# Kernel optimization log

Hardware: AMD Instinct MI355X
Metric: run time of the kernel (lower is better)

## Reference

```python
import jax, jax.numpy as jnp
import numpy as np

D_M, D_K, D_V, HEADS = 1024, 64, 64, 16
B, S = 2, 2048


def setup_inputs() -> dict:
    key = jax.random.key(0)
    ks = jax.random.split(key, 5)
    x = jax.random.normal(ks[0], (B, S, D_M), dtype=jnp.float32)
    # per-head projection weights (original deep-copies one rand init per head;
    # we give each head independent weights, matching the per-head param structure)
    Wk = jax.random.uniform(ks[1], (HEADS, D_M, D_K), dtype=jnp.float32)
    Wq = jax.random.uniform(ks[2], (HEADS, D_M, D_K), dtype=jnp.float32)
    Wv = jax.random.uniform(ks[3], (HEADS, D_M, D_V), dtype=jnp.float32)
    Wo = jax.random.uniform(ks[4], (HEADS * D_V, D_M), dtype=jnp.float32)
    return {"x": x, "Wk": Wk, "Wq": Wq, "Wv": Wv, "Wo": Wo}


def reference(x, Wk, Wq, Wv, Wo):
    # per-head QKV projections, batched over heads: [B,H,S,d]
    q = jnp.einsum("bsm,hmk->bhsk", x, Wq)
    k = jnp.einsum("bsm,hmk->bhsk", x, Wk)
    v = jnp.einsum("bsm,hmv->bhsv", x, Wv)
    scale = 1.0 / jnp.sqrt(jnp.asarray(q.shape[-1], dtype=q.dtype))
    scores = jnp.einsum("bhsk,bhtk->bhst", q, k) * scale  # [B,H,S,S]
    attn = jax.nn.softmax(scores, axis=-1)
    ctx = jnp.einsum("bhst,bhtv->bhsv", attn, v)  # [B,H,S,d_v]
    # concat heads -> [B,S,H*d_v], then output projection
    ctx = jnp.transpose(ctx, (0, 2, 1, 3)).reshape(x.shape[0], x.shape[1], -1)
    return jnp.einsum("bsc,cm->bsm", ctx, Wo)
```

## Files before the change

kernel.cpp:

```cpp
#include <hip/hip_runtime.h>
#include <hip/hip_bf16.h>
#include <stdint.h>

#define DM   1024
#define DKV  64
#define HEADS 16
#define BATCH 2
#define SEQ  2048
#define BS   (BATCH*SEQ)
#define BHD  (BATCH*HEADS)

typedef __attribute__((ext_vector_type(8))) short bf16x8;
typedef __attribute__((ext_vector_type(4))) short bf16x4;
typedef __attribute__((ext_vector_type(4))) float f32x4;

__device__ inline unsigned fb(float f) { union { float f; unsigned u; } v; v.f = f; return v.u; }

__device__ inline unsigned short bf16_rtn(float f) {
  unsigned u = fb(f);
  unsigned r = u + 0x7fffu + ((u >> 16) & 1u);
  return (unsigned short)(r >> 16);
}
__device__ inline float bf16_to_f(unsigned short h) {
  union { unsigned u; float f; } v; v.u = ((unsigned)h) << 16; return v.f;
}
__device__ inline void split_bf16(float x, unsigned short& hi, unsigned short& lo) {
  hi = bf16_rtn(x);
  lo = bf16_rtn(x - bf16_to_f(hi));
}
__device__ inline unsigned pack2_bf16(float lo_elem, float hi_elem) {
  return __builtin_amdgcn_perm(fb(hi_elem) + 0x8000u, fb(lo_elem) + 0x8000u, 0x07060302u);
}

__device__ inline float fast_exp2(float x) {
#if __has_builtin(__builtin_amdgcn_exp2f)
  return __builtin_amdgcn_exp2f(x);
#else
  return exp2f(x);
#endif
}

__device__ inline f32x4 mfma16x16x16_bf16(bf16x4 a, bf16x4 b, f32x4 c) {
#if __has_builtin(__builtin_amdgcn_mfma_f32_16x16x16bf16_1k)
  return __builtin_amdgcn_mfma_f32_16x16x16bf16_1k(a, b, c, 0, 0, 0);
#else
  asm volatile("v_mfma_f32_16x16x16_bf16 %0, %1, %2, %0" : "+v"(c) : "v"(a), "v"(b));
  return c;
#endif
}

__device__ inline void stage16(const unsigned short* g, unsigned short* lds_base, int lane) {
#if __has_builtin(__builtin_amdgcn_global_load_lds)
  __builtin_amdgcn_global_load_lds((__attribute__((address_space(1))) void*)(g),
                                   (__attribute__((address_space(3))) void*)(lds_base),
                                   16, 0, 0);
#else
  *(bf16x8*)(lds_base + lane * 8) = *(const bf16x8*)g;
#endif
}

__device__ inline int swz(int row, int chunk) {
  return row * 64 + (((chunk ^ (row & 7)) & 7) << 3);
}

__global__ void cvt_x_split(const float* __restrict__ x,
                            unsigned short* __restrict__ xh, unsigned short* __restrict__ xl) {
  int i = (blockIdx.x * 256 + threadIdx.x) * 8;
  bf16x8 oh, ol;
  #pragma unroll
  for (int j = 0; j < 8; ++j) {
    unsigned short hi, lo;
    split_bf16(x[i + j], hi, lo);
    oh[j] = (short)hi; ol[j] = (short)lo;
  }
  *(bf16x8*)(xh + i) = oh;
  *(bf16x8*)(xl + i) = ol;
}

__global__ void pack_qkv_split(const float* __restrict__ Wq, const float* __restrict__ Wk,
                               const float* __restrict__ Wv,
                               unsigned short* __restrict__ Wh, unsigned short* __restrict__ Wl) {
  __shared__ float tile[64][65];
  int bid = blockIdx.x;
  int p = bid >> 8, h = (bid >> 4) & 15, mt = bid & 15;
  const float* W = (p == 0) ? Wq : (p == 1) ? Wk : Wv;
  const float* src = W + (size_t)h * (DM * DKV);
  int t = threadIdx.x;
  int m0 = mt * 64;
  #pragma unroll
  for (int pass = 0; pass < 16; ++pass) {
    int row = pass * 4 + (t >> 6), col = t & 63;
    tile[row][col] = src[(size_t)(m0 + row) * DKV + col];
  }
  __syncthreads();
  int cbase = p * 1024 + h * 64;
  #pragma unroll
  for (int pass = 0; pass < 16; ++pass) {
    int krow = pass * 4 + (t >> 6), mcol = t & 63;
    unsigned short hi, lo;
    split_bf16(tile[mcol][krow], hi, lo);
    size_t idx = (size_t)(cbase + krow) * DM + m0 + mcol;
    Wh[idx] = hi; Wl[idx] = lo;
  }
}

__global__ void pack_wo(const float* __restrict__ Wo, unsigned short* __restrict__ WoT) {
  __shared__ float tile[64][65];
  int ib = blockIdx.x >> 4, jb = blockIdx.x & 15;
  int t = threadIdx.x;
  #pragma unroll
  for (int pass = 0; pass < 16; ++pass) {
    int row = pass * 4 + (t >> 6), col = t & 63;
    tile[row][col] = Wo[(size_t)(ib * 64 + row) * DM + jb * 64 + col];
  }
  __syncthreads();
  #pragma unroll
  for (int pass = 0; pass < 16; ++pass) {
    int a = pass * 4 + (t >> 6), b = t & 63;
    WoT[(size_t)(jb * 64 + a) * DM + ib * 64 + b] = bf16_rtn(tile[b][a]);
  }
}

__global__ __launch_bounds__(256, 2)
void gemm_qk(const unsigned short* __restrict__ Ah, const unsigned short* __restrict__ Al,
             const unsigned short* __restrict__ Bh, const unsigned short* __restrict__ Bl,
             unsigned short* __restrict__ Qh, unsigned short* __restrict__ Ql,
             unsigned short* __restrict__ Kh, unsigned short* __restrict__ Kl) {
  __shared__ unsigned short AsH[128 * 32], AsL[128 * 32];
  __shared__ unsigned short BsH[128 * 32], BsL[128 * 32];
  const int tid = threadIdx.x;
  const int w = tid >> 6, lane = tid & 63;
  const int quad = lane >> 4, l16 = lane & 15;
  const int wm = w >> 1, wn = w & 1;
  const int bn = blockIdx.x, bm = blockIdx.y;

  f32x4 acc[4][4];
  #pragma unroll
  for (int i = 0; i < 4; ++i)
    #pragma unroll
    for (int j = 0; j < 4; ++j) acc[i][j] = (f32x4){0.f, 0.f, 0.f, 0.f};

  const int r4 = lane >> 2, c4 = lane & 3;
  const size_t offA = (size_t)(bm * 128 + w * 32 + r4) * DM + c4 * 8;
  const size_t offB = (size_t)(bn * 128 + w * 32 + r4) * DM + c4 * 8;
  unsigned short* lAh0 = AsH + (w * 32) * 32;      unsigned short* lAh1 = AsH + (w * 32 + 16) * 32;
  unsigned short* lAl0 = AsL + (w * 32) * 32;      unsigned short* lAl1 = AsL + (w * 32 + 16) * 32;
  unsigned short* lBh0 = BsH + (w * 32) * 32;      unsigned short* lBh1 = BsH + (w * 32 + 16) * 32;
  unsigned short* lBl0 = BsL + (w * 32) * 32;      unsigned short* lBl1 = BsL + (w * 32 + 16) * 32;

  for (int kk = 0; kk < DM / 32; ++kk) {
    stage16(Ah + offA + kk * 32,           lAh0, lane);
    stage16(Ah + offA + kk * 32 + 16 * DM, lAh1, lane);
    stage16(Al + offA + kk * 32,           lAl0, lane);
    stage16(Al + offA + kk * 32 + 16 * DM, lAl1, lane);
    stage16(Bh + offB + kk * 32,           lBh0, lane);
    stage16(Bh + offB + kk * 32 + 16 * DM, lBh1, lane);
    stage16(Bl + offB + kk * 32,           lBl0, lane);
    stage16(Bl + offB + kk * 32 + 16 * DM, lBl1, lane);
    asm volatile("s_waitcnt vmcnt(0)" ::: "memory");
    __syncthreads();
    bf16x8 afh[4], afl[4], bfh[4], bfl[4];
    #pragma unroll
    for (int mt = 0; mt < 4; ++mt) {
      afh[mt] = *(const bf16x8*)(AsH + (wm * 64 + mt * 16 + l16) * 32 + quad * 8);
      afl[mt] = *(const bf16x8*)(AsL + (wm * 64 + mt * 16 + l16) * 32 + quad * 8);
    }
    #pragma unroll
    for (int nt = 0; nt < 4; ++nt) {
      bfh[nt] = *(const bf16x8*)(BsH + (wn * 64 + nt * 16 + l16) * 32 + quad * 8);
      bfl[nt] = *(const bf16x8*)(BsL + (wn * 64 + nt * 16 + l16) * 32 + quad * 8);
    }
    #pragma unroll
    for (int mt = 0; mt < 4; ++mt)
      #pragma unroll
      for (int nt = 0; nt < 4; ++nt) {
        acc[mt][nt] = __builtin_amdgcn_mfma_f32_16x16x32_bf16(afh[mt], bfh[nt], acc[mt][nt], 0, 0, 0);
        acc[mt][nt] = __builtin_amdgcn_mfma_f32_16x16x32_bf16(afh[mt], bfl[nt], acc[mt][nt], 0, 0, 0);
        acc[mt][nt] = __builtin_amdgcn_mfma_f32_16x16x32_bf16(afl[mt], bfh[nt], acc[mt][nt], 0, 0, 0);
      }
    __syncthreads();
  }

  const float SCL = 0.18033688011112042f;
  #pragma unroll
  for (int mt = 0; mt < 4; ++mt) {
    int m_g = bm * 128 + wm * 64 + mt * 16 + quad * 4;
    #pragma unroll
    for (int nt = 0; nt < 4; ++nt) {
      int n_g = bn * 128 + wn * 64 + nt * 16 + l16;
      int p = n_g >> 10, h = (n_g >> 6) & 15, k = n_g & 63;
      #pragma unroll
      for (int r = 0; r < 4; ++r) {
        int row = m_g + r;
        int b = row >> 11, s = row & 2047;
        int bh = b * HEADS + h;
        float v = acc[mt][nt][r];
        size_t idx = ((size_t)(bh * SEQ + s)) * DKV + k;
        unsigned short hi, lo;
        if (p == 0) {
          split_bf16(v * SCL, hi, lo);
          Qh[idx] = hi; Ql[idx] = lo;
        } else {
          split_bf16(v, hi, lo);
          Kh[idx] = hi; Kl[idx] = lo;
        }
      }
    }
  }
}

__global__ __launch_bounds__(256, 2)
void gemm_v(const unsigned short* __restrict__ A, const unsigned short* __restrict__ Bt,
            unsigned short* __restrict__ Vt) {
  __shared__ unsigned short As[128 * 32];
  __shared__ unsigned short Bs[128 * 32];
  const int tid = threadIdx.x;
  const int w = tid >> 6, lane = tid & 63;
  const int quad = lane >> 4, l16 = lane & 15;
  const int wm = w >> 1, wn = w & 1;
  const int bn = blockIdx.x, bm = blockIdx.y;

  f32x4 acc[4][4];
  #pragma unroll
  for (int i = 0; i < 4; ++i)
    #pragma unroll
    for (int j = 0; j < 4; ++j) acc[i][j] = (f32x4){0.f, 0.f, 0.f, 0.f};

  const int r4 = lane >> 2, c4 = lane & 3;
  const unsigned short* gA0 = A  + (size_t)(bm * 128 + w * 32 + r4) * DM + c4 * 8;
  const unsigned short* gB0 = Bt + (size_t)(bn * 128 + w * 32 + r4) * DM + c4 * 8;
  unsigned short* lA0 = As + (w * 32) * 32;
  unsigned short* lA1 = As + (w * 32 + 16) * 32;
  unsigned short* lB0 = Bs + (w * 32) * 32;
  unsigned short* lB1 = Bs + (w * 32 + 16) * 32;

  for (int kk = 0; kk < DM / 32; ++kk) {
    stage16(gA0 + kk * 32,           lA0, lane);
    stage16(gA0 + kk * 32 + 16 * DM, lA1, lane);
    stage16(gB0 + kk * 32,           lB0, lane);
    stage16(gB0 + kk * 32 + 16 * DM, lB1, lane);
    asm volatile("s_waitcnt vmcnt(0)" ::: "memory");
    __syncthreads();
    bf16x8 af[4], bfr[4];
    #pragma unroll
    for (int mt = 0; mt < 4; ++mt)
      af[mt] = *(const bf16x8*)(As + (wm * 64 + mt * 16 + l16) * 32 + quad * 8);
    #pragma unroll
    for (int nt = 0; nt < 4; ++nt)
      bfr[nt] = *(const bf16x8*)(Bs + (wn * 64 + nt * 16 + l16) * 32 + quad * 8);
    #pragma unroll
    for (int mt = 0; mt < 4; ++mt)
      #pragma unroll
      for (int nt = 0; nt < 4; ++nt)
        acc[mt][nt] = __builtin_amdgcn_mfma_f32_16x16x32_bf16(af[mt], bfr[nt], acc[mt][nt], 0, 0, 0);
    __syncthreads();
  }

  #pragma unroll
  for (int mt = 0; mt < 4; ++mt) {
    int m_g = bm * 128 + wm * 64 + mt * 16 + quad * 4;
    #pragma unroll
    for (int nt = 0; nt < 4; ++nt) {
      int n_g = bn * 128 + wn * 64 + nt * 16 + l16;
      int h = n_g >> 6, k = n_g & 63;
      #pragma unroll
      for (int r = 0; r < 4; ++r) {
        int row = m_g + r;
        int b = row >> 11, s = row & 2047;
        int bh = b * HEADS + h;
        Vt[((size_t)(bh * DKV + k)) * SEQ + s] = bf16_rtn(acc[mt][nt][r]);
      }
    }
  }
}

__global__ __launch_bounds__(256, 2)
void flash(const unsigned short* __restrict__ Qh, const unsigned short* __restrict__ Ql,
           const unsigned short* __restrict__ Kh, const unsigned short* __restrict__ Kl,
           const unsigned short* __restrict__ Vt, unsigned short* __restrict__ ctx) {
  __shared__ unsigned short KtH[64 * 64], KtL[64 * 64], Vts[64 * 64];
  const int tid = threadIdx.x;
  const int w = tid >> 6, lane = tid & 63, quad = lane >> 4, l16 = lane & 15;
  const int bh = blockIdx.x;
  const int q0 = blockIdx.y * 128;

  bf16x8 qfh[2][2], qfl[2][2];
  #pragma unroll
  for (int qt = 0; qt < 2; ++qt) {
    int qrow = q0 + w * 32 + qt * 16 + l16;
    size_t base = ((size_t)(bh * SEQ + qrow)) * DKV + quad * 8;
    qfh[qt][0] = *(const bf16x8*)(Qh + base);
    qfh[qt][1] = *(const bf16x8*)(Qh + base + 32);
    qfl[qt][0] = *(const bf16x8*)(Ql + base);
    qfl[qt][1] = *(const bf16x8*)(Ql + base + 32);
  }

  float m_run[2] = {-1e30f, -1e30f};
  float l_run[2] = {0.f, 0.f};
  f32x4 acc[2][4];
  #pragma unroll
  for (int qt = 0; qt < 2; ++qt)
    #pragma unroll
    for (int vt = 0; vt < 4; ++vt) acc[qt][vt] = (f32x4){0.f, 0.f, 0.f, 0.f};

  const int srow = tid >> 3, sc8 = tid & 7;

  bf16x8 rkh[2], rkl[2], rv[2];
  #pragma unroll
  for (int p = 0; p < 2; ++p) {
    int row = p * 32 + srow;
    size_t kidx = ((size_t)(bh * SEQ + row)) * DKV + sc8 * 8;
    rkh[p] = *(const bf16x8*)(Kh + kidx);
    rkl[p] = *(const bf16x8*)(Kl + kidx);
    rv[p]  = *(const bf16x8*)(Vt + ((size_t)(bh * DKV + row)) * SEQ + sc8 * 8);
  }

  for (int kt = 0; kt < SEQ / 64; ++kt) {
    __syncthreads();
    #pragma unroll
    for (int p = 0; p < 2; ++p) {
      int row = p * 32 + srow;
      int o = swz(row, sc8);
      *(bf16x8*)(KtH + o) = rkh[p];
      *(bf16x8*)(KtL + o) = rkl[p];
      *(bf16x8*)(Vts + o) = rv[p];
    }
    __syncthreads();
    if (kt + 1 < SEQ / 64) {
      int kt0 = (kt + 1) * 64;
      #pragma unroll
      for (int p = 0; p < 2; ++p) {
        int row = p * 32 + srow;
        size_t kidx = ((size_t)(bh * SEQ + kt0 + row)) * DKV + sc8 * 8;
        rkh[p] = *(const bf16x8*)(Kh + kidx);
        rkl[p] = *(const bf16x8*)(Kl + kidx);
        rv[p]  = *(const bf16x8*)(Vt + ((size_t)(bh * DKV + row)) * SEQ + kt0 + sc8 * 8);
      }
    }

    f32x4 st[4][2];
    #pragma unroll
    for (int mt = 0; mt < 4; ++mt) {
      int rowA = mt * 16 + l16;
      bf16x8 kah0 = *(const bf16x8*)(KtH + swz(rowA, quad));
      bf16x8 kah1 = *(const bf16x8*)(KtH + swz(rowA, quad + 4));
      bf16x8 kal0 = *(const bf16x8*)(KtL + swz(rowA, quad));
      bf16x8 kal1 = *(const bf16x8*)(KtL + swz(rowA, quad + 4));
      #pragma unroll
      for (int qt = 0; qt < 2; ++qt) {
        f32x4 c = (f32x4){0.f, 0.f, 0.f, 0.f};
        c = __builtin_amdgcn_mfma_f32_16x16x32_bf16(kah0, qfh[qt][0], c, 0, 0, 0);
        c = __builtin_amdgcn_mfma_f32_16x16x32_bf16(kah1, qfh[qt][1], c, 0, 0, 0);
        c = __builtin_amdgcn_mfma_f32_16x16x32_bf16(kah0, qfl[qt][0], c, 0, 0, 0);
        c = __builtin_amdgcn_mfma_f32_16x16x32_bf16(kah1, qfl[qt][1], c, 0, 0, 0);
        c = __builtin_amdgcn_mfma_f32_16x16x32_bf16(kal0, qfh[qt][0], c, 0, 0, 0);
        c = __builtin_amdgcn_mfma_f32_16x16x32_bf16(kal1, qfh[qt][1], c, 0, 0, 0);
        st[mt][qt] = c;
      }
    }

    bf16x4 pb[2][4];
    #pragma unroll
    for (int qt = 0; qt < 2; ++qt) {
      float cm = -1e30f;
      #pragma unroll
      for (int mt = 0; mt < 4; ++mt)
        #pragma unroll
        for (int r = 0; r < 4; ++r) cm = fmaxf(cm, st[mt][qt][r]);
      cm = fmaxf(cm, __shfl_xor(cm, 16));
      cm = fmaxf(cm, __shfl_xor(cm, 32));
      bool upd = cm > m_run[qt];
      float mn = upd ? cm : m_run[qt];
      float ssum = 0.f;
      #pragma unroll
      for (int mt = 0; mt < 4; ++mt) {
        float p0 = fast_exp2(st[mt][qt][0] - mn);
        float p1 = fast_exp2(st[mt][qt][1] - mn);
        float p2 = fast_exp2(st[mt][qt][2] - mn);
        float p3 = fast_exp2(st[mt][qt][3] - mn);
        ssum += (p0 + p1) + (p2 + p3);
        union { bf16x4 v; unsigned u2[2]; } pk;
        pk.u2[0] = pack2_bf16(p0, p1);
        pk.u2[1] = pack2_bf16(p2, p3);
        pb[qt][mt] = pk.v;
      }
      ssum += __shfl_xor(ssum, 16);
      ssum += __shfl_xor(ssum, 32);
      if (__ballot(upd)) {
        float alpha = fast_exp2(m_run[qt] - mn);
        m_run[qt] = mn;
        l_run[qt] = l_run[qt] * alpha + ssum;
        #pragma unroll
        for (int vt = 0; vt < 4; ++vt) acc[qt][vt] = acc[qt][vt] * alpha;
      } else {
        l_run[qt] += ssum;
      }
    }

    #pragma unroll
    for (int vt = 0; vt < 4; ++vt) {
      #pragma unroll
      for (int mt = 0; mt < 4; ++mt) {
        int row = vt * 16 + l16;
        int addr = row * 64 + ((((mt * 2 + (quad >> 1)) ^ (row & 7)) & 7) << 3) + (quad & 1) * 4;
        bf16x4 va = *(const bf16x4*)(Vts + addr);
        #pragma unroll
        for (int qt = 0; qt < 2; ++qt)
          acc[qt][vt] = mfma16x16x16_bf16(va, pb[qt][mt], acc[qt][vt]);
      }
    }
  }

  int h = bh & 15, b = bh >> 4;
  #pragma unroll
  for (int qt = 0; qt < 2; ++qt) {
    float inv = 1.0f / l_run[qt];
    int bs = b * SEQ + q0 + w * 32 + qt * 16 + l16;
    #pragma unroll
    for (int vt = 0; vt < 4; ++vt) {
      union { bf16x4 v; unsigned u2[2]; } pk;
      pk.u2[0] = pack2_bf16(acc[qt][vt][0] * inv, acc[qt][vt][1] * inv);
      pk.u2[1] = pack2_bf16(acc[qt][vt][2] * inv, acc[qt][vt][3] * inv);
      *(bf16x4*)(ctx + (size_t)bs * DM + h * 64 + vt * 16 + quad * 4) = pk.v;
    }
  }
}

__global__ __launch_bounds__(256, 2)
void gemm_out(const unsigned short* __restrict__ A, const unsigned short* __restrict__ Bt,
              float* __restrict__ out) {
  __shared__ unsigned short As[128 * 32];
  __shared__ unsigned short Bs[128 * 32];
  const int tid = threadIdx.x;
  const int w = tid >> 6, lane = tid & 63;
  const int quad = lane >> 4, l16 = lane & 15;
  const int wm = w >> 1, wn = w & 1;
  const int bn = blockIdx.x, bm = blockIdx.y;

  f32x4 acc[4][4];
  #pragma unroll
  for (int i = 0; i < 4; ++i)
    #pragma unroll
    for (int j = 0; j < 4; ++j) acc[i][j] = (f32x4){0.f, 0.f, 0.f, 0.f};

  const int r4 = lane >> 2, c4 = lane & 3;
  const unsigned short* gA0 = A  + (size_t)(bm * 128 + w * 32 + r4) * DM + c4 * 8;
  const unsigned short* gB0 = Bt + (size_t)(bn * 128 + w * 32 + r4) * DM + c4 * 8;
  unsigned short* lA0 = As + (w * 32) * 32;
  unsigned short* lA1 = As + (w * 32 + 16) * 32;
  unsigned short* lB0 = Bs + (w * 32) * 32;
  unsigned short* lB1 = Bs + (w * 32 + 16) * 32;

  for (int kk = 0; kk < DM / 32; ++kk) {
    stage16(gA0 + kk * 32,           lA0, lane);
    stage16(gA0 + kk * 32 + 16 * DM, lA1, lane);
    stage16(gB0 + kk * 32,           lB0, lane);
    stage16(gB0 + kk * 32 + 16 * DM, lB1, lane);
    asm volatile("s_waitcnt vmcnt(0)" ::: "memory");
    __syncthreads();
    bf16x8 af[4], bfr[4];
    #pragma unroll
    for (int mt = 0; mt < 4; ++mt)
      af[mt] = *(const bf16x8*)(As + (wm * 64 + mt * 16 + l16) * 32 + quad * 8);
    #pragma unroll
    for (int nt = 0; nt < 4; ++nt)
      bfr[nt] = *(const bf16x8*)(Bs + (wn * 64 + nt * 16 + l16) * 32 + quad * 8);
    #pragma unroll
    for (int mt = 0; mt < 4; ++mt)
      #pragma unroll
      for (int nt = 0; nt < 4; ++nt)
        acc[mt][nt] = __builtin_amdgcn_mfma_f32_16x16x32_bf16(af[mt], bfr[nt], acc[mt][nt], 0, 0, 0);
    __syncthreads();
  }

  #pragma unroll
  for (int mt = 0; mt < 4; ++mt) {
    int m_g = bm * 128 + wm * 64 + mt * 16 + quad * 4;
    #pragma unroll
    for (int nt = 0; nt < 4; ++nt) {
      int n_g = bn * 128 + wn * 64 + nt * 16 + l16;
      #pragma unroll
      for (int r = 0; r < 4; ++r)
        out[(size_t)(m_g + r) * DM + n_g] = acc[mt][nt][r];
    }
  }
}

extern "C" void kernel_launch(void* const* d_in, const int* in_sizes, int n_in,
                              void* d_out, int out_size, void* d_ws, size_t ws_size,
                              hipStream_t stream) {
  const float* x  = (const float*)d_in[0];
  const float* Wk = (const float*)d_in[1];
  const float* Wq = (const float*)d_in[2];
  const float* Wv = (const float*)d_in[3];
  const float* Wo = (const float*)d_in[4];
  float* out = (float*)d_out;

  unsigned short* xh  = (unsigned short*)d_ws;
  unsigned short* xl  = xh  + (size_t)BS * DM;
  unsigned short* Wh  = xl  + (size_t)BS * DM;
  unsigned short* Wl  = Wh  + (size_t)3 * DM * DM;
  unsigned short* WoT = Wl  + (size_t)3 * DM * DM;
  unsigned short* Qh  = WoT + (size_t)DM * DM;
  unsigned short* Ql  = Qh  + (size_t)BHD * SEQ * DKV;
  unsigned short* Kh  = Ql  + (size_t)BHD * SEQ * DKV;
  unsigned short* Kl  = Kh  + (size_t)BHD * SEQ * DKV;
  unsigned short* Vtb = Kl  + (size_t)BHD * SEQ * DKV;
  unsigned short* ctx = Vtb + (size_t)BHD * SEQ * DKV;

  cvt_x_split<<<(BS * DM) / (256 * 8), 256, 0, stream>>>(x, xh, xl);
  pack_qkv_split<<<3 * 16 * 16, 256, 0, stream>>>(Wq, Wk, Wv, Wh, Wl);
  pack_wo<<<16 * 16, 256, 0, stream>>>(Wo, WoT);
  gemm_qk<<<dim3(16, 32), 256, 0, stream>>>(xh, xl, Wh, Wl, Qh, Ql, Kh, Kl);
  gemm_v<<<dim3(8, 32), 256, 0, stream>>>(xh, Wh + (size_t)2048 * DM, Vtb);
  flash<<<dim3(BHD, SEQ / 128), 256, 0, stream>>>(Qh, Ql, Kh, Kl, Vtb, ctx);
  gemm_out<<<dim3(8, 32), 256, 0, stream>>>(ctx, WoT, out);
}
```

Before: 270.8 us.

## Load K and V MFMA fragments directly from global memory, dropping LDS staging

The flash kernel no longer stages K (hi/lo) and V tiles through shared memory with two barriers per iteration. Each wave now loads its own MFMA operand fragments for K and V straight from global memory into registers, prefetching the next tile after the current use. This removes the LDS writes, LDS reads and __syncthreads. In exchange, each of the four waves fetches the full K/V tile on its own, using fewer, narrower accesses, which multiplies global/L2 traffic and adds register pressure.

```diff
diff --git a/kernel.cpp b/kernel.cpp
--- a/kernel.cpp
+++ b/kernel.cpp
@@ -57,10 +57,6 @@
 #else
   *(bf16x8*)(lds_base + lane * 8) = *(const bf16x8*)g;
 #endif
-}
-
-__device__ inline int swz(int row, int chunk) {
-  return row * 64 + (((chunk ^ (row & 7)) & 7) << 3);
 }
 
 __global__ void cvt_x_split(const float* __restrict__ x,
@@ -278,7 +274,6 @@
 void flash(const unsigned short* __restrict__ Qh, const unsigned short* __restrict__ Ql,
            const unsigned short* __restrict__ Kh, const unsigned short* __restrict__ Kl,
            const unsigned short* __restrict__ Vt, unsigned short* __restrict__ ctx) {
-  __shared__ unsigned short KtH[64 * 64], KtL[64 * 64], Vts[64 * 64];
   const int tid = threadIdx.x;
   const int w = tid >> 6, lane = tid & 63, quad = lane >> 4, l16 = lane & 15;
   const int bh = blockIdx.x;
@@ -303,59 +298,52 @@
     #pragma unroll
     for (int vt = 0; vt < 4; ++vt) acc[qt][vt] = (f32x4){0.f, 0.f, 0.f, 0.f};
 
-  const int srow = tid >> 3, sc8 = tid & 7;
-
-  bf16x8 rkh[2], rkl[2], rv[2];
-  #pragma unroll
-  for (int p = 0; p < 2; ++p) {
-    int row = p * 32 + srow;
-    size_t kidx = ((size_t)(bh * SEQ + row)) * DKV + sc8 * 8;
-    rkh[p] = *(const bf16x8*)(Kh + kidx);
-    rkl[p] = *(const bf16x8*)(Kl + kidx);
-    rv[p]  = *(const bf16x8*)(Vt + ((size_t)(bh * DKV + row)) * SEQ + sc8 * 8);
-  }
+  const size_t krow0 = ((size_t)(bh * SEQ + l16)) * DKV + quad * 8;
+  const size_t vrow0 = ((size_t)(bh * DKV + l16)) * SEQ + quad * 4;
+
+  bf16x8 kfh[4][2], kfl[4][2];
+  bf16x4 vf[4][4];
+
+  #pragma unroll
+  for (int mt = 0; mt < 4; ++mt) {
+    size_t r = krow0 + (size_t)(mt * 16) * DKV;
+    kfh[mt][0] = *(const bf16x8*)(Kh + r);
+    kfh[mt][1] = *(const bf16x8*)(Kh + r + 32);
+    kfl[mt][0] = *(const bf16x8*)(Kl + r);
+    kfl[mt][1] = *(const bf16x8*)(Kl + r + 32);
+  }
+  #pragma unroll
+  for (int vt = 0; vt < 4; ++vt)
+    #pragma unroll
+    for (int mt = 0; mt < 4; ++mt)
+      vf[vt][mt] = *(const bf16x4*)(Vt + vrow0 + (size_t)(vt * 16) * SEQ + mt * 16);
 
   for (int kt = 0; kt < SEQ / 64; ++kt) {
-    __syncthreads();
-    #pragma unroll
-    for (int p = 0; p < 2; ++p) {
-      int row = p * 32 + srow;
-      int o = swz(row, sc8);
-      *(bf16x8*)(KtH + o) = rkh[p];
-      *(bf16x8*)(KtL + o) = rkl[p];
-      *(bf16x8*)(Vts + o) = rv[p];
-    }
-    __syncthreads();
-    if (kt + 1 < SEQ / 64) {
-      int kt0 = (kt + 1) * 64;
-      #pragma unroll
-      for (int p = 0; p < 2; ++p) {
-        int row = p * 32 + srow;
-        size_t kidx = ((size_t)(bh * SEQ + kt0 + row)) * DKV + sc8 * 8;
-        rkh[p] = *(const bf16x8*)(Kh + kidx);
-        rkl[p] = *(const bf16x8*)(Kl + kidx);
-        rv[p]  = *(const bf16x8*)(Vt + ((size_t)(bh * DKV + row)) * SEQ + kt0 + sc8 * 8);
-      }
-    }
-
     f32x4 st[4][2];
     #pragma unroll
     for (int mt = 0; mt < 4; ++mt) {
-      int rowA = mt * 16 + l16;
-      bf16x8 kah0 = *(const bf16x8*)(KtH + swz(rowA, quad));
-      bf16x8 kah1 = *(const bf16x8*)(KtH + swz(rowA, quad + 4));
-      bf16x8 kal0 = *(const bf16x8*)(KtL + swz(rowA, quad));
-      bf16x8 kal1 = *(const bf16x8*)(KtL + swz(rowA, quad + 4));
       #pragma unroll
       for (int qt = 0; qt < 2; ++qt) {
         f32x4 c = (f32x4){0.f, 0.f, 0.f, 0.f};
-        c = __builtin_amdgcn_mfma_f32_16x16x32_bf16(kah0, qfh[qt][0], c, 0, 0, 0);
-        c = __builtin_amdgcn_mfma_f32_16x16x32_bf16(kah1, qfh[qt][1], c, 0, 0, 0);
-        c = __builtin_amdgcn_mfma_f32_16x16x32_bf16(kah0, qfl[qt][0], c, 0, 0, 0);
-        c = __builtin_amdgcn_mfma_f32_16x16x32_bf16(kah1, qfl[qt][1], c, 0, 0, 0);
-        c = __builtin_amdgcn_mfma_f32_16x16x32_bf16(kal0, qfh[qt][0], c, 0, 0, 0);
-        c = __builtin_amdgcn_mfma_f32_16x16x32_bf16(kal1, qfh[qt][1], c, 0, 0, 0);
+        c = __builtin_amdgcn_mfma_f32_16x16x32_bf16(kfh[mt][0], qfh[qt][0], c, 0, 0, 0);
+        c = __builtin_amdgcn_mfma_f32_16x16x32_bf16(kfh[mt][1], qfh[qt][1], c, 0, 0, 0);
+        c = __builtin_amdgcn_mfma_f32_16x16x32_bf16(kfh[mt][0], qfl[qt][0], c, 0, 0, 0);
+        c = __builtin_amdgcn_mfma_f32_16x16x32_bf16(kfh[mt][1], qfl[qt][1], c, 0, 0, 0);
+        c = __builtin_amdgcn_mfma_f32_16x16x32_bf16(kfl[mt][0], qfh[qt][0], c, 0, 0, 0);
+        c = __builtin_amdgcn_mfma_f32_16x16x32_bf16(kfl[mt][1], qfh[qt][1], c, 0, 0, 0);
         st[mt][qt] = c;
+      }
+    }
+
+    if (kt + 1 < SEQ / 64) {
+      size_t kbase = krow0 + (size_t)((kt + 1) * 64) * DKV;
+      #pragma unroll
+      for (int mt = 0; mt < 4; ++mt) {
+        size_t r = kbase + (size_t)(mt * 16) * DKV;
+        kfh[mt][0] = *(const bf16x8*)(Kh + r);
+        kfh[mt][1] = *(const bf16x8*)(Kh + r + 32);
+        kfl[mt][0] = *(const bf16x8*)(Kl + r);
+        kfl[mt][1] = *(const bf16x8*)(Kl + r + 32);
       }
     }
 
@@ -398,16 +386,20 @@
     }
 
     #pragma unroll
-    for (int vt = 0; vt < 4; ++vt) {
-      #pragma unroll
-      for (int mt = 0; mt < 4; ++mt) {
-        int row = vt * 16 + l16;
-        int addr = row * 64 + ((((mt * 2 + (quad >> 1)) ^ (row & 7)) & 7) << 3) + (quad & 1) * 4;
-        bf16x4 va = *(const bf16x4*)(Vts + addr);
+    for (int vt = 0; vt < 4; ++vt)
+      #pragma unroll
+      for (int mt = 0; mt < 4; ++mt)
         #pragma unroll
         for (int qt = 0; qt < 2; ++qt)
-          acc[qt][vt] = mfma16x16x16_bf16(va, pb[qt][mt], acc[qt][vt]);
-      }
+          acc[qt][vt] = mfma16x16x16_bf16(vf[vt][mt], pb[qt][mt], acc[qt][vt]);
+
+    if (kt + 1 < SEQ / 64) {
+      size_t vbase = vrow0 + (kt + 1) * 64;
+      #pragma unroll
+      for (int vt = 0; vt < 4; ++vt)
+        #pragma unroll
+        for (int mt = 0; mt < 4; ++mt)
+          vf[vt][mt] = *(const bf16x4*)(Vt + vbase + (size_t)(vt * 16) * SEQ + mt * 16);
     }
   }
 
```

Measured after the change: 417.2 us. 1.54x slower.

## Split flash attention KV sequence across two warp groups with in-block merge

Applied to the files above, without the earlier changes.

The flash kernel now launches 512 threads per block. Two groups of four waves each process half of the key/value sequence for the same 128 query rows, each with its own shared-memory tiles. At the end the first group writes its partial accumulators and running max/sum to shared memory, and the second group merges them with rescaling before writing ctx. This doubles per-block parallelism to hide latency, on a grid of only 512 blocks, at the cost of more shared memory, a merge step and extra barriers. The launch bound asks for 4 blocks of 512 threads, which may force register spilling.

```diff
diff --git a/kernel.cpp b/kernel.cpp
--- a/kernel.cpp
+++ b/kernel.cpp
@@ -274,20 +274,28 @@
   }
 }
 
-__global__ __launch_bounds__(256, 2)
+__global__ __launch_bounds__(512, 4)
 void flash(const unsigned short* __restrict__ Qh, const unsigned short* __restrict__ Ql,
            const unsigned short* __restrict__ Kh, const unsigned short* __restrict__ Kl,
            const unsigned short* __restrict__ Vt, unsigned short* __restrict__ ctx) {
-  __shared__ unsigned short KtH[64 * 64], KtL[64 * 64], Vts[64 * 64];
+  __shared__ unsigned short smem[24576];
+  __shared__ float mlbuf[4][2][16][2];
   const int tid = threadIdx.x;
   const int w = tid >> 6, lane = tid & 63, quad = lane >> 4, l16 = lane & 15;
+  const int kh = w >> 2;
+  const int qw = w & 3;
   const int bh = blockIdx.x;
   const int q0 = blockIdx.y * 128;
+  const int kbase = kh * (SEQ / 2);
+
+  unsigned short* KtH = smem + kh * 12288;
+  unsigned short* KtL = KtH + 4096;
+  unsigned short* Vts = KtH + 8192;
 
   bf16x8 qfh[2][2], qfl[2][2];
   #pragma unroll
   for (int qt = 0; qt < 2; ++qt) {
-    int qrow = q0 + w * 32 + qt * 16 + l16;
+    int qrow = q0 + qw * 32 + qt * 16 + l16;
     size_t base = ((size_t)(bh * SEQ + qrow)) * DKV + quad * 8;
     qfh[qt][0] = *(const bf16x8*)(Qh + base);
     qfh[qt][1] = *(const bf16x8*)(Qh + base + 32);
@@ -303,19 +311,20 @@
     #pragma unroll
     for (int vt = 0; vt < 4; ++vt) acc[qt][vt] = (f32x4){0.f, 0.f, 0.f, 0.f};
 
-  const int srow = tid >> 3, sc8 = tid & 7;
+  const int tid_h = (qw << 6) | lane;
+  const int srow = tid_h >> 3, sc8 = tid_h & 7;
 
   bf16x8 rkh[2], rkl[2], rv[2];
   #pragma unroll
   for (int p = 0; p < 2; ++p) {
     int row = p * 32 + srow;
-    size_t kidx = ((size_t)(bh * SEQ + row)) * DKV + sc8 * 8;
+    size_t kidx = ((size_t)(bh * SEQ + kbase + row)) * DKV + sc8 * 8;
     rkh[p] = *(const bf16x8*)(Kh + kidx);
     rkl[p] = *(const bf16x8*)(Kl + kidx);
-    rv[p]  = *(const bf16x8*)(Vt + ((size_t)(bh * DKV + row)) * SEQ + sc8 * 8);
-  }
-
-  for (int kt = 0; kt < SEQ / 64; ++kt) {
+    rv[p]  = *(const bf16x8*)(Vt + ((size_t)(bh * DKV + row)) * SEQ + kbase + sc8 * 8);
+  }
+
+  for (int kt = 0; kt < SEQ / 128; ++kt) {
     __syncthreads();
     #pragma unroll
     for (int p = 0; p < 2; ++p) {
@@ -326,8 +335,8 @@
       *(bf16x8*)(Vts + o) = rv[p];
     }
     __syncthreads();
-    if (kt + 1 < SEQ / 64) {
-      int kt0 = (kt + 1) * 64;
+    if (kt + 1 < SEQ / 128) {
+      int kt0 = kbase + (kt + 1) * 64;
       #pragma unroll
       for (int p = 0; p < 2; ++p) {
         int row = p * 32 + srow;
@@ -411,17 +420,44 @@
     }
   }
 
-  int h = bh & 15, b = bh >> 4;
-  #pragma unroll
-  for (int qt = 0; qt < 2; ++qt) {
-    float inv = 1.0f / l_run[qt];
-    int bs = b * SEQ + q0 + w * 32 + qt * 16 + l16;
-    #pragma unroll
-    for (int vt = 0; vt < 4; ++vt) {
-      union { bf16x4 v; unsigned u2[2]; } pk;
-      pk.u2[0] = pack2_bf16(acc[qt][vt][0] * inv, acc[qt][vt][1] * inv);
-      pk.u2[1] = pack2_bf16(acc[qt][vt][2] * inv, acc[qt][vt][3] * inv);
-      *(bf16x4*)(ctx + (size_t)bs * DM + h * 64 + vt * 16 + quad * 4) = pk.v;
+  __syncthreads();
+  float* pbuf = (float*)smem;
+  const int slot = ((qw << 6) | lane) * 36;
+  if (kh == 0) {
+    #pragma unroll
+    for (int qt = 0; qt < 2; ++qt) {
+      #pragma unroll
+      for (int vt = 0; vt < 4; ++vt)
+        *(f32x4*)(pbuf + slot + (qt * 4 + vt) * 4) = acc[qt][vt];
+      if (quad == 0) {
+        mlbuf[qw][qt][l16][0] = m_run[qt];
+        mlbuf[qw][qt][l16][1] = l_run[qt];
+      }
+    }
+  }
+  __syncthreads();
+  if (kh == 1) {
+    int h = bh & 15, b = bh >> 4;
+    #pragma unroll
+    for (int qt = 0; qt < 2; ++qt) {
+      float mA = mlbuf[qw][qt][l16][0], lA = mlbuf[qw][qt][l16][1];
+      float mm = fmaxf(mA, m_run[qt]);
+      float aA = fast_exp2(mA - mm), aB = fast_exp2(m_run[qt] - mm);
+      float inv = 1.0f / (lA * aA + l_run[qt] * aB);
+      float sA = aA * inv, sB = aB * inv;
+      int bs = b * SEQ + q0 + qw * 32 + qt * 16 + l16;
+      #pragma unroll
+      for (int vt = 0; vt < 4; ++vt) {
+        f32x4 oA = *(const f32x4*)(pbuf + slot + (qt * 4 + vt) * 4);
+        float o0 = oA[0] * sA + acc[qt][vt][0] * sB;
+        float o1 = oA[1] * sA + acc[qt][vt][1] * sB;
+        float o2 = oA[2] * sA + acc[qt][vt][2] * sB;
+        float o3 = oA[3] * sA + acc[qt][vt][3] * sB;
+        union { bf16x4 v; unsigned u2[2]; } pk;
+        pk.u2[0] = pack2_bf16(o0, o1);
+        pk.u2[1] = pack2_bf16(o2, o3);
+        *(bf16x4*)(ctx + (size_t)bs * DM + h * 64 + vt * 16 + quad * 4) = pk.v;
+      }
     }
   }
 }
@@ -513,6 +549,6 @@
   pack_wo<<<16 * 16, 256, 0, stream>>>(Wo, WoT);
   gemm_qk<<<dim3(16, 32), 256, 0, stream>>>(xh, xl, Wh, Wl, Qh, Ql, Kh, Kl);
   gemm_v<<<dim3(8, 32), 256, 0, stream>>>(xh, Wh + (size_t)2048 * DM, Vtb);
-  flash<<<dim3(BHD, SEQ / 128), 256, 0, stream>>>(Qh, Ql, Kh, Kl, Vtb, ctx);
+  flash<<<dim3(BHD, SEQ / 128), 512, 0, stream>>>(Qh, Ql, Kh, Kl, Vtb, ctx);
   gemm_out<<<dim3(8, 32), 256, 0, stream>>>(ctx, WoT, out);
 }
```

After: 354.1 us. 1.31x slower.
